# Kernel tuning notes

Measured on AMD Instinct MI355X. Metric: run time of the kernel, lower is better.

Reference implementation:

```python
import jax, jax.numpy as jnp
import numpy as np

B, S = 64, 64
IMG_F, EMB, HID, VOCAB = 2048, 512, 512, 32000


def setup_inputs() -> dict:
    key = jax.random.key(0)
    ks = jax.random.split(key, 12)
    s = 0.02
    return {
        "img": jax.random.normal(ks[0], (B, IMG_F), jnp.float32),
        "captions": jax.random.randint(ks[1], (B, S), 0, VOCAB),
        "embed_W": jax.random.normal(ks[2], (VOCAB, EMB), jnp.float32) * s,
        "Wi": jax.random.normal(ks[3], (IMG_F, HID), jnp.float32) * s,
        "bi": jax.random.normal(ks[4], (HID,), jnp.float32) * s,
        "Wx": jax.random.normal(ks[5], (EMB, HID), jnp.float32) * s,
        "bx": jax.random.normal(ks[6], (HID,), jnp.float32) * s,
        "Wh": jax.random.normal(ks[7], (HID, HID), jnp.float32) * s,
        "bh": jax.random.normal(ks[8], (HID, HID)[:1] + (HID,), jnp.float32)[0] * s if False else jax.random.normal(ks[8], (HID,), jnp.float32) * s,
        "Wy": jax.random.normal(ks[9], (HID, VOCAB), jnp.float32) * s,
        "by": jax.random.normal(ks[10], (VOCAB,), jnp.float32) * s,
    }


def reference(img, captions, embed_W, Wi, bi, Wx, bx, Wh, bh, Wy, by):
    # Embed caption inputs (drop last token): (B, T, EMB), T = S-1
    x = embed_W[captions[:, :-1]]
    # Precompute input-to-hidden preactivations for all steps: (B, T, HID)
    pre = jnp.einsum("bte,eh->bth", x, Wx) + bx
    # Image features are injected only at t=0 (as in the torch loop)
    pre = pre.at[:, 0].add(img @ Wi + bi)

    def step(h_prev, p_t):
        h_t = jnp.tanh(p_t + h_prev @ Wh + bh)
        return h_t, h_t

    h0 = jnp.zeros((img.shape[0], Wh.shape[0]), dtype=x.dtype)
    _, hs = jax.lax.scan(step, h0, pre.transpose(1, 0, 2))  # (T, B, HID)
    hs = hs.transpose(1, 0, 2)  # (B, T, HID)
    # Output projection in one big GEMM (same math as per-step h2y)
    logits = jnp.einsum("bth,hv->btv", hs, Wy) + by  # (B, T, VOCAB)
    return logits
```

## Files before the change

kernel.cpp:

```cpp
#include <hip/hip_runtime.h>
#include <hip/hip_bf16.h>

#define B_    64
#define S_    64
#define T_    63
#define IMGF  2048
#define EMB   512
#define HID   512
#define VOCAB 32000
#define MROWS 4032
#define MPAD  4096

typedef __bf16 bf16;
typedef __bf16 bf16x8 __attribute__((ext_vector_type(8)));
typedef float  f32x4  __attribute__((ext_vector_type(4)));

__device__ __forceinline__ void gload_lds16(const void* g, void* l) {
  __builtin_amdgcn_global_load_lds(
      (const __attribute__((address_space(1))) unsigned int*)g,
      (__attribute__((address_space(3))) unsigned int*)l, 16, 0, 0);
}

#define LGKM_BARRIER() asm volatile("s_waitcnt lgkmcnt(0)\n\ts_barrier" ::: "memory")

__global__ __launch_bounds__(256) void transpose_w(
    const float* __restrict__ W, bf16* __restrict__ WT, int K, int N)
{
  __shared__ float tile[64][65];
  const int tx = threadIdx.x & 63, ty = threadIdx.x >> 6;
  const int n0 = blockIdx.x * 64, k0 = blockIdx.y * 64;
  #pragma unroll
  for (int r = ty; r < 64; r += 4)
    tile[r][tx] = W[(size_t)(k0 + r) * N + n0 + tx];
  __syncthreads();
  #pragma unroll
  for (int r = ty; r < 64; r += 4)
    WT[(size_t)(n0 + r) * K + k0 + tx] = (bf16)tile[tx][r];
}

__global__ __launch_bounds__(256) void embed_gather(
    const float* __restrict__ embW, const int* __restrict__ captions,
    bf16* __restrict__ X)
{
  const int r = blockIdx.x;
  const int tid = threadIdx.x;
  if (r < MROWS) {
    const int b = r / T_, t = r % T_;
    const int idx = captions[b * S_ + t];
    float2 v = ((const float2*)(embW + (size_t)idx * EMB))[tid];
    X[(size_t)r * EMB + 2 * tid]     = (bf16)v.x;
    X[(size_t)r * EMB + 2 * tid + 1] = (bf16)v.y;
  } else {
    X[(size_t)r * EMB + 2 * tid]     = (bf16)0.f;
    X[(size_t)r * EMB + 2 * tid + 1] = (bf16)0.f;
  }
}

__global__ __launch_bounds__(256) void img_to_bf16(
    const float* __restrict__ img, bf16* __restrict__ imgB)
{
  const int r = blockIdx.x;
  const int tid = threadIdx.x;
  #pragma unroll
  for (int j = 0; j < 8; j++) {
    const int c = tid + j * 256;
    const float v = (r < B_) ? img[(size_t)r * IMGF + c] : 0.f;
    imgB[(size_t)r * IMGF + c] = (bf16)v;
  }
}

__global__ __launch_bounds__(256) void gemm_bt(
    const bf16* __restrict__ A, const bf16* __restrict__ BT,
    const float* __restrict__ bias, float* __restrict__ C,
    int Mvalid, int N, int K)
{
  __shared__ __align__(16) bf16 As[2][128 * 32];
  __shared__ __align__(16) bf16 Bs[2][128 * 32];
  const int tid  = threadIdx.x;
  const int wave = tid >> 6, lane = tid & 63;
  const int wm = wave >> 1, wn = wave & 1;
  const int bm = blockIdx.x, bn = blockIdx.y;
  const int lg = lane >> 4, lr = lane & 15;

  f32x4 acc[4][4];
  #pragma unroll
  for (int m = 0; m < 4; m++)
    #pragma unroll
    for (int n = 0; n < 4; n++) acc[m][n] = (f32x4){0.f, 0.f, 0.f, 0.f};

  const bf16* Abase = A  + (size_t)bm * 128 * K;
  const bf16* Bbase = BT + (size_t)bn * 128 * K;

  const int c0 = wave * 64 + lane;
  const int r0 = c0 >> 2,  sl0 = (c0 & 3) ^ ((r0 >> 1) & 3);
  const int c1 = 256 + c0;
  const int r1 = c1 >> 2,  sl1 = (c1 & 3) ^ ((r1 >> 1) & 3);

  const int NT = K >> 5;

#define STAGE_TILE(buf, kt)                                                   \
  do {                                                                        \
    gload_lds16(Abase + (size_t)r0 * K + (kt) + sl0 * 8,                      \
                &As[buf][(wave * 64) * 8]);                                   \
    gload_lds16(Abase + (size_t)r1 * K + (kt) + sl1 * 8,                      \
                &As[buf][(256 + wave * 64) * 8]);                             \
    gload_lds16(Bbase + (size_t)r0 * K + (kt) + sl0 * 8,                      \
                &Bs[buf][(wave * 64) * 8]);                                   \
    gload_lds16(Bbase + (size_t)r1 * K + (kt) + sl1 * 8,                      \
                &Bs[buf][(256 + wave * 64) * 8]);                             \
  } while (0)

  STAGE_TILE(0, 0);
  int cur = 0;
  for (int it = 0; it < NT; ++it) {
    __syncthreads();
    if (it + 1 < NT) STAGE_TILE(cur ^ 1, (it + 1) * 32);

    bf16x8 af[4], bfr[4];
    #pragma unroll
    for (int m = 0; m < 4; m++) {
      const int r = wm * 64 + m * 16 + lr;
      const int sp = lg ^ ((r >> 1) & 3);
      af[m] = *(const bf16x8*)&As[cur][r * 32 + sp * 8];
    }
    #pragma unroll
    for (int n = 0; n < 4; n++) {
      const int r = wn * 64 + n * 16 + lr;
      const int sp = lg ^ ((r >> 1) & 3);
      bfr[n] = *(const bf16x8*)&Bs[cur][r * 32 + sp * 8];
    }
    #pragma unroll
    for (int m = 0; m < 4; m++)
      #pragma unroll
      for (int n = 0; n < 4; n++)
        acc[m][n] = __builtin_amdgcn_mfma_f32_16x16x32_bf16(af[m], bfr[n], acc[m][n], 0, 0, 0);
    cur ^= 1;
  }
#undef STAGE_TILE

  const int row0 = bm * 128 + wm * 64 + (lane >> 4) * 4;
  const int col0 = bn * 128 + wn * 64 + lr;
  #pragma unroll
  for (int m = 0; m < 4; m++) {
    #pragma unroll
    for (int n = 0; n < 4; n++) {
      const int col = col0 + n * 16;
      const float bv = bias[col];
      #pragma unroll
      for (int q = 0; q < 4; q++) {
        const int row = row0 + m * 16 + q;
        if (row < Mvalid) C[(size_t)row * N + col] = acc[m][n][q] + bv;
      }
    }
  }
}

#define FREG 48
#define FLDS 16
__global__ __launch_bounds__(512, 1) void rnn_reg8(
    const float* __restrict__ pre, const bf16* __restrict__ WhT,
    const float* __restrict__ bh, const float* __restrict__ pimg,
    bf16* __restrict__ hs)
{
  const int bg  = blockIdx.x;
  const int tid = threadIdx.x;
  const int wave = tid >> 6, lane = tid & 63;
  const int lg = lane >> 4, lr = lane & 15;
  const int gb0 = bg * 16;
  const int wc0 = wave * 64;

  __shared__ __align__(16) bf16 hsh[16 * 512];
  __shared__ __align__(16) bf16 bls[8 * FLDS * 64 * 8];

  bf16x8 bw[FREG];
  #pragma unroll
  for (int f = 0; f < 64; f++) {
    const int n = f >> 4, kf = f & 15;
    const bf16x8 v = *(const bf16x8*)(WhT + (size_t)(wc0 + n * 16 + lr) * 512
                                          + kf * 32 + lg * 8);
    if (f < FREG) bw[f] = v;
    else *(bf16x8*)&bls[((wave * FLDS + (f - FREG)) * 64 + lane) * 8] = v;
  }

  *(f32x4*)&hsh[tid * 16]     = (f32x4){0.f, 0.f, 0.f, 0.f};
  *(f32x4*)&hsh[tid * 16 + 8] = (f32x4){0.f, 0.f, 0.f, 0.f};

  float bhv[4];
  #pragma unroll
  for (int n = 0; n < 4; n++) bhv[n] = bh[wc0 + n * 16 + lr];
  const float* preb = pre + ((size_t)(gb0 + lg * 4) * T_) * 512 + wc0 + lr;

  __syncthreads();

  #pragma unroll 1
  for (int t = 0; t < T_; t++) {
    float prq[4][4];
    #pragma unroll
    for (int n = 0; n < 4; n++)
      #pragma unroll
      for (int q = 0; q < 4; q++)
        prq[n][q] = preb[(size_t)q * (T_ * 512) + (size_t)t * 512 + n * 16];

    f32x4 acc[4];
    #pragma unroll
    for (int n = 0; n < 4; n++) acc[n] = (f32x4){0.f, 0.f, 0.f, 0.f};

    #pragma unroll
    for (int kf = 0; kf < 16; kf++) {
      const int c = (kf * 4 + lg) ^ (lr & 7);
      const bf16x8 a = *(const bf16x8*)&hsh[(lr * 64 + c) * 8];
      #pragma unroll
      for (int n = 0; n < 4; n++) {
        const int f = n * 16 + kf;
        bf16x8 bfrag;
        if (f < FREG) bfrag = bw[f];
        else bfrag = *(const bf16x8*)&bls[((wave * FLDS + (f - FREG)) * 64 + lane) * 8];
        acc[n] = __builtin_amdgcn_mfma_f32_16x16x32_bf16(a, bfrag, acc[n], 0, 0, 0);
      }
    }
    LGKM_BARRIER();

    #pragma unroll
    for (int n = 0; n < 4; n++) {
      #pragma unroll
      for (int q = 0; q < 4; q++) {
        const int bl = lg * 4 + q;
        const int b  = gb0 + bl;
        const int k  = wc0 + n * 16 + lr;
        float s = acc[n][q] + prq[n][q] + bhv[n];
        if (t == 0) s += pimg[(size_t)b * HID + k];
        const float e = __builtin_exp2f(s * 2.885390081777927f);
        const float hv = 1.f - 2.f * __builtin_amdgcn_rcpf(e + 1.f);
        hs[((size_t)b * T_ + t) * HID + k] = (bf16)hv;
        const int c = (k >> 3) ^ (bl & 7);
        hsh[bl * 512 + c * 8 + (k & 7)] = (bf16)hv;
      }
    }
    LGKM_BARRIER();
  }
}

extern "C" void kernel_launch(void* const* d_in, const int* in_sizes, int n_in,
                              void* d_out, int out_size, void* d_ws, size_t ws_size,
                              hipStream_t stream) {
  const float* img      = (const float*)d_in[0];
  const int*   captions = (const int*)d_in[1];
  const float* embW     = (const float*)d_in[2];
  const float* Wi       = (const float*)d_in[3];
  const float* bi       = (const float*)d_in[4];
  const float* Wx       = (const float*)d_in[5];
  const float* bx       = (const float*)d_in[6];
  const float* Wh       = (const float*)d_in[7];
  const float* bh       = (const float*)d_in[8];
  const float* Wy       = (const float*)d_in[9];
  const float* by       = (const float*)d_in[10];
  float* logits = (float*)d_out;

  char* ws = (char*)d_ws;
  bf16*  WyT  = (bf16*)(ws);
  bf16*  WxT  = (bf16*)(ws + 32768000);
  bf16*  X    = (bf16*)(ws + 33292288);
  bf16*  hs   = (bf16*)(ws + 37486592);
  float* pre  = (float*)(ws + 41680896);
  float* pimg = (float*)(ws + 49938432);
  bf16*  imgB = (bf16*)(ws + 50200576);
  bf16*  WiT  = (bf16*)(ws + 50724864);
  bf16*  WhT  = WxT;

  transpose_w<<<dim3(VOCAB / 64, HID / 64), 256, 0, stream>>>(Wy, WyT, HID, VOCAB);
  transpose_w<<<dim3(HID / 64, EMB / 64), 256, 0, stream>>>(Wx, WxT, EMB, HID);
  transpose_w<<<dim3(HID / 64, IMGF / 64), 256, 0, stream>>>(Wi, WiT, IMGF, HID);
  img_to_bf16<<<128, 256, 0, stream>>>(img, imgB);

  embed_gather<<<MPAD, 256, 0, stream>>>(embW, captions, X);

  gemm_bt<<<dim3(MPAD / 128, HID / 128), 256, 0, stream>>>(X, WxT, bx, pre, MROWS, HID, HID);

  gemm_bt<<<dim3(1, HID / 128), 256, 0, stream>>>(imgB, WiT, bi, pimg, B_, HID, IMGF);

  transpose_w<<<dim3(HID / 64, HID / 64), 256, 0, stream>>>(Wh, WhT, HID, HID);

  hipMemsetAsync(hs + (size_t)MROWS * HID, 0,
                 (size_t)(MPAD - MROWS) * HID * sizeof(bf16), stream);

  rnn_reg8<<<4, 512, 0, stream>>>(pre, WhT, bh, pimg, hs);

  gemm_bt<<<dim3(MPAD / 128, VOCAB / 128), 256, 0, stream>>>(hs, WyT, by, logits, MROWS, VOCAB, HID);
}
```

Baseline: 679.9 us.

## Use 256x256-tile, 4-stage pipelined GEMM for the vocab output projection

Adds a new GEMM kernel with 256x256 output tiles, 512 threads (8 waves, each computing 128x64), and a 4-buffer LDS ring that keeps three K-stages in flight using vmcnt-based waits. It replaces the 128x128 double-buffered GEMM for the large hidden-to-vocab projection. The goal is more operand reuse per LDS load and better hiding of global-load latency. In exchange it uses more LDS and registers (one block per CU) and launches fewer blocks (16x125), which may leave CUs unevenly loaded.

After: 646.4 us. -4.9%, faster.

```diff
diff --git a/kernel.cpp b/kernel.cpp
--- a/kernel.cpp
+++ b/kernel.cpp
@@ -142,6 +142,97 @@
   const int col0 = bn * 128 + wn * 64 + lr;
   #pragma unroll
   for (int m = 0; m < 4; m++) {
+    #pragma unroll
+    for (int n = 0; n < 4; n++) {
+      const int col = col0 + n * 16;
+      const float bv = bias[col];
+      #pragma unroll
+      for (int q = 0; q < 4; q++) {
+        const int row = row0 + m * 16 + q;
+        if (row < Mvalid) C[(size_t)row * N + col] = acc[m][n][q] + bv;
+      }
+    }
+  }
+}
+
+__global__ __launch_bounds__(512, 1) void gemm_bt256(
+    const bf16* __restrict__ A, const bf16* __restrict__ BT,
+    const float* __restrict__ bias, float* __restrict__ C,
+    int Mvalid, int N, int K)
+{
+  __shared__ __align__(16) bf16 sm[4][2][256 * 32];
+  const int tid  = threadIdx.x;
+  const int wave = tid >> 6, lane = tid & 63;
+  const int wm = wave >> 2, wn = wave & 3;
+  const int bm = blockIdx.x, bn = blockIdx.y;
+  const int lg = lane >> 4, lr = lane & 15;
+
+  f32x4 acc[8][4];
+  #pragma unroll
+  for (int m = 0; m < 8; m++)
+    #pragma unroll
+    for (int n = 0; n < 4; n++) acc[m][n] = (f32x4){0.f, 0.f, 0.f, 0.f};
+
+  const bf16* Abase = A  + (size_t)bm * 256 * K;
+  const bf16* Bbase = BT + (size_t)bn * 256 * K;
+
+  const int ca0 = tid,        ra0 = ca0 >> 2, sa0 = (ca0 & 3) ^ (ra0 & 3);
+  const int ca1 = tid + 512,  ra1 = ca1 >> 2, sa1 = (ca1 & 3) ^ (ra1 & 3);
+  const int ldsb0 = (wave * 64) * 8;
+  const int ldsb1 = (512 + wave * 64) * 8;
+
+#define STAGE256(buf, kt)                                                     \
+  do {                                                                        \
+    gload_lds16(Abase + (size_t)ra0 * K + (kt) + sa0 * 8, &sm[buf][0][ldsb0]);\
+    gload_lds16(Abase + (size_t)ra1 * K + (kt) + sa1 * 8, &sm[buf][0][ldsb1]);\
+    gload_lds16(Bbase + (size_t)ra0 * K + (kt) + sa0 * 8, &sm[buf][1][ldsb0]);\
+    gload_lds16(Bbase + (size_t)ra1 * K + (kt) + sa1 * 8, &sm[buf][1][ldsb1]);\
+  } while (0)
+
+  const int NT = K >> 5;
+  STAGE256(0, 0);
+  STAGE256(1, 32);
+  STAGE256(2, 64);
+
+  #pragma unroll 1
+  for (int it = 0; it < NT; ++it) {
+    const int newer = (NT - 1 - it) > 2 ? 2 : (NT - 1 - it);
+    switch (newer) {
+      case 2:  asm volatile("s_waitcnt vmcnt(8)\n\ts_barrier" ::: "memory"); break;
+      case 1:  asm volatile("s_waitcnt vmcnt(4)\n\ts_barrier" ::: "memory"); break;
+      default: asm volatile("s_waitcnt vmcnt(0)\n\ts_barrier" ::: "memory"); break;
+    }
+
+    const bf16* As_ = sm[it & 3][0];
+    const bf16* Bs_ = sm[it & 3][1];
+    bf16x8 af[8], bfr[4];
+    #pragma unroll
+    for (int m = 0; m < 8; m++) {
+      const int r = wm * 128 + m * 16 + lr;
+      const int sp = lg ^ (r & 3);
+      af[m] = *(const bf16x8*)&As_[(r * 4 + sp) * 8];
+    }
+    #pragma unroll
+    for (int n = 0; n < 4; n++) {
+      const int r = wn * 64 + n * 16 + lr;
+      const int sp = lg ^ (r & 3);
+      bfr[n] = *(const bf16x8*)&Bs_[(r * 4 + sp) * 8];
+    }
+    #pragma unroll
+    for (int m = 0; m < 8; m++)
+      #pragma unroll
+      for (int n = 0; n < 4; n++)
+        acc[m][n] = __builtin_amdgcn_mfma_f32_16x16x32_bf16(af[m], bfr[n], acc[m][n], 0, 0, 0);
+
+    LGKM_BARRIER();
+    if (it + 3 < NT) STAGE256((it + 3) & 3, (it + 3) * 32);
+  }
+#undef STAGE256
+
+  const int row0 = bm * 256 + wm * 128 + lg * 4;
+  const int col0 = bn * 256 + wn * 64 + lr;
+  #pragma unroll
+  for (int m = 0; m < 8; m++) {
     #pragma unroll
     for (int n = 0; n < 4; n++) {
       const int col = col0 + n * 16;
@@ -285,5 +376,5 @@
 
   rnn_reg8<<<4, 512, 0, stream>>>(pre, WhT, bh, pimg, hs);
 
-  gemm_bt<<<dim3(MPAD / 128, VOCAB / 128), 256, 0, stream>>>(hs, WyT, by, logits, MROWS, VOCAB, HID);
-}
+  gemm_bt256<<<dim3(MPAD / 256, VOCAB / 256), 512, 0, stream>>>(hs, WyT, by, logits, MROWS, VOCAB, HID);
+}
```
